# Optimization experiments

Hardware: AMD Instinct MI355X
Metric: run time of the kernel (lower is better)

Reference implementation:

```python
import jax, jax.numpy as jnp
import numpy as np

N_NODES = 50000
HIDDEN = 128
N_EDGES = 1_600_000


def gcn_conv(x, W, b, src, dst, n_nodes):
    """PyG GCNConv: linear, add self-loops, symmetric deg^-1/2 normalization, scatter-sum."""
    h = x @ W  # [N, D]
    # degree with self-loops: 1 + in-degree from edges (edge weight 1)
    deg = jnp.ones((n_nodes,), h.dtype).at[dst].add(1.0)
    dinv = jax.lax.rsqrt(deg)  # deg^{-1/2}, deg >= 1 so no inf
    # neighbor messages: norm_e = dinv[src] * dinv[dst]
    msgs = h[src] * (dinv[src] * dinv[dst])[:, None]  # [E, D]
    agg = jnp.zeros_like(h).at[dst].add(msgs)
    # self-loop contribution: norm = dinv[i]*dinv[i]
    agg = agg + h * (dinv * dinv)[:, None]
    return agg + b


def setup_inputs() -> dict:
    key = jax.random.key(0)
    ks = jax.random.split(key, 7)
    x = jax.random.normal(ks[0], (N_NODES, HIDDEN), dtype=jnp.float32)
    edge_index = jax.random.randint(ks[1], (2, N_EDGES), 0, N_NODES, dtype=jnp.int64)
    s = 1.0 / np.sqrt(HIDDEN)
    W1 = jax.random.uniform(ks[2], (HIDDEN, HIDDEN), jnp.float32, -s, s)
    b1 = jax.random.uniform(ks[3], (HIDDEN,), jnp.float32, -s, s)
    W2 = jax.random.uniform(ks[4], (HIDDEN, HIDDEN), jnp.float32, -s, s)
    b2 = jax.random.uniform(ks[5], (HIDDEN,), jnp.float32, -s, s)
    return {"x": x, "edge_index": edge_index, "W1": W1, "b1": b1, "W2": W2, "b2": b2}


def reference(x, edge_index, W1, b1, W2, b2):
    src, dst = edge_index[0], edge_index[1]
    h = jax.nn.relu(gcn_conv(x, W1, b1, src, dst, N_NODES))
    z = gcn_conv(h, W2, b2, src, dst, N_NODES)
    return z
```

## Files before the change

kernel.cpp:

```cpp
#include <hip/hip_runtime.h>
#include <hip/hip_fp16.h>
#include <type_traits>

#define D 128
#define NI 256
#define MAXNW 25024

using half8 = __attribute__((ext_vector_type(8))) _Float16;
using f32x4 = __attribute__((ext_vector_type(4))) float;


__global__ __launch_bounds__(256) void wprep_kernel(const float* __restrict__ W1,
                                                    const float* __restrict__ W2,
                                                    __half* __restrict__ Wt1,
                                                    __half* __restrict__ Wt2) {
  const float* W = blockIdx.x ? W2 : W1;
  __half* Wt = blockIdx.x ? Wt2 : Wt1;
  for (int idx = threadIdx.x; idx < D * D; idx += 256) {
    int c = idx & 127, k = idx >> 7;
    Wt[c * D + k] = __float2half(W[k * D + c]);
  }
}


__global__ __launch_bounds__(1024) void histA_kernel(const int* __restrict__ dst,
                                                     unsigned short* __restrict__ c,
                                                     unsigned short* __restrict__ rank,
                                                     int E, int N, int CH) {
  __shared__ unsigned int cnt[MAXNW];
  int i = blockIdx.x;
  int nw = (N + 1) >> 1;
  for (int k = threadIdx.x; k < nw; k += 1024) cnt[k] = 0u;
  __syncthreads();
  int e0 = i * CH, e1 = min(e0 + CH, E);
  for (int e = e0 + (int)threadIdx.x; e < e1; e += 1024) {
    int d = dst[e];
    int sh = (d & 1) * 16;
    unsigned int old = atomicAdd(&cnt[d >> 1], 1u << sh);
    rank[e] = (unsigned short)((old >> sh) & 0xffffu);
  }
  __syncthreads();
  unsigned short* ci = c + (size_t)i * N;
  if ((N & 1) == 0) {
    unsigned int* ci32 = reinterpret_cast<unsigned int*>(ci);
    for (int k = threadIdx.x; k < nw; k += 1024) ci32[k] = cnt[k];
  } else {
    for (int k = threadIdx.x; k < nw; k += 1024) {
      unsigned int v = cnt[k];
      int n0 = k * 2;
      ci[n0] = (unsigned short)(v & 0xffffu);
      if (n0 + 1 < N) ci[n0 + 1] = (unsigned short)(v >> 16);
    }
  }
}


__global__ __launch_bounds__(256) void histB_kernel(unsigned short* __restrict__ c,
                                                    int* __restrict__ deg, int N) {
  int n = blockIdx.x * 256 + threadIdx.x;
  if (n >= N) return;
  int run = 0;
  #pragma unroll 8
  for (int i = 0; i < NI; ++i) {
    size_t idx = (size_t)i * N + n;
    int v = c[idx];
    c[idx] = (unsigned short)run;
    run += v;
  }
  deg[n] = run;
}


__global__ __launch_bounds__(256) void bsum_kernel(const int* __restrict__ deg,
                                                   int* __restrict__ bsum) {
  __shared__ int ws[4];
  int i0 = blockIdx.x * 1024 + threadIdx.x * 4;
  int4 v = *reinterpret_cast<const int4*>(deg + i0);
  int s = v.x + v.y + v.z + v.w;
  #pragma unroll
  for (int off = 32; off; off >>= 1) s += __shfl_down(s, off);
  if ((threadIdx.x & 63) == 0) ws[threadIdx.x >> 6] = s;
  __syncthreads();
  if (threadIdx.x == 0) bsum[blockIdx.x] = ws[0] + ws[1] + ws[2] + ws[3];
}


__global__ __launch_bounds__(256) void scan_kernel(const int* __restrict__ deg,
                                                   const int* __restrict__ bsum,
                                                   int* __restrict__ offsets,
                                                   float* __restrict__ dinv,
                                                   int N, int E) {
  __shared__ int ts[256];
  int b = blockIdx.x;
  int base = 0;
  for (int t = 0; t < b; ++t) base += bsum[t];

  int i0 = b * 1024 + threadIdx.x * 4;
  int4 v = *reinterpret_cast<const int4*>(deg + i0);
  int t4 = v.x + v.y + v.z + v.w;
  ts[threadIdx.x] = t4;
  __syncthreads();
  #pragma unroll
  for (int off = 1; off < 256; off <<= 1) {
    int u = (threadIdx.x >= off) ? ts[threadIdx.x - off] : 0;
    __syncthreads();
    ts[threadIdx.x] += u;
    __syncthreads();
  }
  int run = base + ts[threadIdx.x] - t4;

  int dd[4] = {v.x, v.y, v.z, v.w};
  #pragma unroll
  for (int k = 0; k < 4; ++k) {
    int i = i0 + k;
    if (i < N) {
      offsets[i] = run;
      dinv[i] = rsqrtf(1.0f + (float)dd[k]);
    }
    run += dd[k];
  }
  if (b == 0 && threadIdx.x == 0) offsets[N] = E;
}


__global__ __launch_bounds__(256) void place_kernel(const int* __restrict__ src,
                                                    const int* __restrict__ dst,
                                                    const unsigned short* __restrict__ rank,
                                                    const unsigned short* __restrict__ c,
                                                    const int* __restrict__ offsets,
                                                    const float* __restrict__ dinv,
                                                    unsigned int* __restrict__ csr,
                                                    int E, int N, int CH) {
  int t = blockIdx.x * 256 + threadIdx.x;
  int e0 = t * 4;
  if (e0 + 4 <= E) {
    int4 s4 = *reinterpret_cast<const int4*>(src + e0);
    int4 d4 = *reinterpret_cast<const int4*>(dst + e0);
    ushort4 r4 = *reinterpret_cast<const ushort4*>(rank + e0);
    int ss[4] = {s4.x, s4.y, s4.z, s4.w};
    int dd[4] = {d4.x, d4.y, d4.z, d4.w};
    int rr[4] = {r4.x, r4.y, r4.z, r4.w};
    int pos[4];
    float w[4];
    #pragma unroll
    for (int k = 0; k < 4; ++k) {
      int i = (e0 + k) / CH;
      pos[k] = offsets[dd[k]] + (int)c[(size_t)i * N + dd[k]] + rr[k];
    }
    #pragma unroll
    for (int k = 0; k < 4; ++k) w[k] = dinv[ss[k]];
    #pragma unroll
    for (int k = 0; k < 4; ++k) {
      unsigned int q = (unsigned int)__float2int_rn(w[k] * 32767.0f);
      csr[pos[k]] = ((unsigned int)ss[k] << 15) | q;
    }
  } else {
    for (int e = e0; e < E; ++e) {
      int s = src[e];
      int d = dst[e];
      int i = e / CH;
      int pos = offsets[d] + (int)c[(size_t)i * N + d] + (int)rank[e];
      unsigned int q = (unsigned int)__float2int_rn(dinv[s] * 32767.0f);
      csr[pos] = ((unsigned int)s << 15) | q;
    }
  }
}


template <typename TI>
__global__ __launch_bounds__(256) void gemm_mfma_kernel(const TI* __restrict__ X,
                                                        const __half* __restrict__ Wt,
                                                        __half* __restrict__ H, int N) {
  int wid = threadIdx.x >> 6;
  int l = threadIdx.x & 63;
  int row0w = blockIdx.x * 64 + wid * 16;
  int arow = row0w + (l & 15);
  int k0 = (l >> 4) * 8;

  half8 A[4];
  #pragma unroll
  for (int kt = 0; kt < 4; ++kt) {
    half8 a = {};
    if (arow < N) {
      if constexpr (std::is_same<TI, float>::value) {
        const float* p = X + (size_t)arow * D + kt * 32 + k0;
        float4 u = *reinterpret_cast<const float4*>(p);
        float4 v = *reinterpret_cast<const float4*>(p + 4);
        a[0] = (_Float16)u.x; a[1] = (_Float16)u.y;
        a[2] = (_Float16)u.z; a[3] = (_Float16)u.w;
        a[4] = (_Float16)v.x; a[5] = (_Float16)v.y;
        a[6] = (_Float16)v.z; a[7] = (_Float16)v.w;
      } else {
        a = *reinterpret_cast<const half8*>((const __half*)X + (size_t)arow * D + kt * 32 + k0);
      }
    }
    A[kt] = a;
  }

  int wrow = row0w + (l >> 4) * 4;
  int col = l & 15;
  #pragma unroll
  for (int ct = 0; ct < 8; ++ct) {
    f32x4 acc = {0.f, 0.f, 0.f, 0.f};
    #pragma unroll
    for (int kt = 0; kt < 4; ++kt) {
      half8 b = *reinterpret_cast<const half8*>(Wt + (size_t)(ct * 16 + col) * D + kt * 32 + k0);
      acc = __builtin_amdgcn_mfma_f32_16x16x32_f16(A[kt], b, acc, 0, 0, 0);
    }
    #pragma unroll
    for (int r = 0; r < 4; ++r) {
      int row = wrow + r;
      if (row < N) H[(size_t)row * D + ct * 16 + col] = __float2half(acc[r]);
    }
  }
}


template <int DO_RELU, typename TO>
__global__ __launch_bounds__(256) void agg_kernel(const __half* __restrict__ H,
                                                  const int* __restrict__ offsets,
                                                  const unsigned int* __restrict__ csr,
                                                  const float* __restrict__ dinv,
                                                  const float* __restrict__ bias,
                                                  TO* __restrict__ out, int N) {
  int n = blockIdx.x * 4 + (threadIdx.x >> 6);
  if (n >= N) return;
  int lane = threadIdx.x & 63;
  int g = lane >> 4;
  int l = lane & 15;

  int beg = offsets[n];
  int end = offsets[n + 1];

  float acc[8];
  #pragma unroll
  for (int k = 0; k < 8; ++k) acc[k] = 0.f;

  const __half* Hl = H + l * 8;

  int j = beg + g;
  for (; j + 12 < end; j += 16) {
    unsigned int p0 = csr[j];
    unsigned int p1 = csr[j + 4];
    unsigned int p2 = csr[j + 8];
    unsigned int p3 = csr[j + 12];
    float m0 = (float)(p0 & 0x7fffu) * (1.0f / 32767.0f);
    float m1 = (float)(p1 & 0x7fffu) * (1.0f / 32767.0f);
    float m2 = (float)(p2 & 0x7fffu) * (1.0f / 32767.0f);
    float m3 = (float)(p3 & 0x7fffu) * (1.0f / 32767.0f);
    uint4 r0 = *reinterpret_cast<const uint4*>(Hl + (size_t)(p0 >> 15) * D);
    uint4 r1 = *reinterpret_cast<const uint4*>(Hl + (size_t)(p1 >> 15) * D);
    uint4 r2 = *reinterpret_cast<const uint4*>(Hl + (size_t)(p2 >> 15) * D);
    uint4 r3 = *reinterpret_cast<const uint4*>(Hl + (size_t)(p3 >> 15) * D);
    const __half2* h0 = reinterpret_cast<const __half2*>(&r0);
    const __half2* h1 = reinterpret_cast<const __half2*>(&r1);
    const __half2* h2 = reinterpret_cast<const __half2*>(&r2);
    const __half2* h3 = reinterpret_cast<const __half2*>(&r3);
    #pragma unroll
    for (int k = 0; k < 4; ++k) {
      float2 f0 = __half22float2(h0[k]);
      float2 f1 = __half22float2(h1[k]);
      float2 f2 = __half22float2(h2[k]);
      float2 f3 = __half22float2(h3[k]);
      acc[2 * k]     = fmaf(f0.x, m0, acc[2 * k]);
      acc[2 * k + 1] = fmaf(f0.y, m0, acc[2 * k + 1]);
      acc[2 * k]     = fmaf(f1.x, m1, acc[2 * k]);
      acc[2 * k + 1] = fmaf(f1.y, m1, acc[2 * k + 1]);
      acc[2 * k]     = fmaf(f2.x, m2, acc[2 * k]);
      acc[2 * k + 1] = fmaf(f2.y, m2, acc[2 * k + 1]);
      acc[2 * k]     = fmaf(f3.x, m3, acc[2 * k]);
      acc[2 * k + 1] = fmaf(f3.y, m3, acc[2 * k + 1]);
    }
  }
  for (; j < end; j += 4) {
    unsigned int p0 = csr[j];
    float m0 = (float)(p0 & 0x7fffu) * (1.0f / 32767.0f);
    uint4 r0 = *reinterpret_cast<const uint4*>(Hl + (size_t)(p0 >> 15) * D);
    const __half2* h0 = reinterpret_cast<const __half2*>(&r0);
    #pragma unroll
    for (int k = 0; k < 4; ++k) {
      float2 f0 = __half22float2(h0[k]);
      acc[2 * k]     = fmaf(f0.x, m0, acc[2 * k]);
      acc[2 * k + 1] = fmaf(f0.y, m0, acc[2 * k + 1]);
    }
  }

  #pragma unroll
  for (int k = 0; k < 8; ++k) {
    acc[k] += __shfl_xor(acc[k], 16);
    acc[k] += __shfl_xor(acc[k], 32);
  }

  if (g == 0) {
    float di = dinv[n];
    uint4 rs = *reinterpret_cast<const uint4*>(Hl + (size_t)n * D);
    const __half2* hs = reinterpret_cast<const __half2*>(&rs);
    float4 bv0 = *reinterpret_cast<const float4*>(bias + l * 8);
    float4 bv1 = *reinterpret_cast<const float4*>(bias + l * 8 + 4);
    float v[8];
    #pragma unroll
    for (int k = 0; k < 4; ++k) {
      float2 f = __half22float2(hs[k]);
      v[2 * k]     = fmaf(di, fmaf(di, f.x, acc[2 * k]), 0.f);
      v[2 * k + 1] = fmaf(di, fmaf(di, f.y, acc[2 * k + 1]), 0.f);
    }
    v[0] += bv0.x; v[1] += bv0.y; v[2] += bv0.z; v[3] += bv0.w;
    v[4] += bv1.x; v[5] += bv1.y; v[6] += bv1.z; v[7] += bv1.w;
    if (DO_RELU) {
      #pragma unroll
      for (int k = 0; k < 8; ++k) v[k] = fmaxf(v[k], 0.f);
    }
    if constexpr (std::is_same<TO, float>::value) {
      float4 o0 = make_float4(v[0], v[1], v[2], v[3]);
      float4 o1 = make_float4(v[4], v[5], v[6], v[7]);
      *reinterpret_cast<float4*>(out + (size_t)n * D + l * 8) = o0;
      *reinterpret_cast<float4*>(out + (size_t)n * D + l * 8 + 4) = o1;
    } else {
      uint4 pk;
      __half2 q0 = __floats2half2_rn(v[0], v[1]);
      __half2 q1 = __floats2half2_rn(v[2], v[3]);
      __half2 q2 = __floats2half2_rn(v[4], v[5]);
      __half2 q3 = __floats2half2_rn(v[6], v[7]);
      pk.x = *reinterpret_cast<unsigned int*>(&q0);
      pk.y = *reinterpret_cast<unsigned int*>(&q1);
      pk.z = *reinterpret_cast<unsigned int*>(&q2);
      pk.w = *reinterpret_cast<unsigned int*>(&q3);
      *reinterpret_cast<uint4*>((__half*)out + (size_t)n * D + l * 8) = pk;
    }
  }
}


extern "C" void kernel_launch(void* const* d_in, const int* in_sizes, int n_in,
                              void* d_out, int out_size, void* d_ws, size_t ws_size,
                              hipStream_t stream) {
  const float* x  = (const float*)d_in[0];
  const int* edge = (const int*)d_in[1];
  const float* W1 = (const float*)d_in[2];
  const float* b1 = (const float*)d_in[3];
  const float* W2 = (const float*)d_in[4];
  const float* b2 = (const float*)d_in[5];
  const int N = in_sizes[0] / D;
  const int E = in_sizes[1] / 2;
  const int* srcp = edge;
  const int* dstp = edge + E;
  float* out = (float*)d_out;

  const int NP = (N + 1023) & ~1023;
  const int SB = NP / 1024;
  const int CH = (E + NI - 1) / NI;

  auto align = [](size_t v) { return (v + 255) & ~(size_t)255; };
  char* ws = (char*)d_ws;
  size_t o = 0;
  int*   deg     = (int*)(ws + o);             o += align((size_t)NP * 4);
  int*   bsum    = (int*)(ws + o);             o += align((size_t)SB * 4);
  int*   offsets = (int*)(ws + o);             o += align((size_t)(N + 1) * 4);
  float* dinv    = (float*)(ws + o);           o += align((size_t)N * 4);
  unsigned short* c    = (unsigned short*)(ws + o); o += align((size_t)NI * N * 2);
  unsigned short* rank = (unsigned short*)(ws + o); o += align((size_t)((E + 3) & ~3) * 2);
  unsigned int* csr = (unsigned int*)(ws + o); o += align((size_t)E * 4);
  __half* Hh     = (__half*)(ws + o);          o += align((size_t)N * D * 2);
  __half* h1h    = (__half*)(ws + o);          o += align((size_t)N * D * 2);
  __half* Wt1    = (__half*)(ws + o);          o += align((size_t)D * D * 2);
  __half* Wt2    = (__half*)(ws + o);          o += align((size_t)D * D * 2);

  int gemm_blocks = (N + 63) / 64;
  int agg_blocks  = (N + 3) / 4;

  hipMemsetAsync(deg, 0, (size_t)NP * 4, stream);
  wprep_kernel<<<2, 256, 0, stream>>>(W1, W2, Wt1, Wt2);
  histA_kernel<<<NI, 1024, 0, stream>>>(dstp, c, rank, E, N, CH);
  histB_kernel<<<(N + 255) / 256, 256, 0, stream>>>(c, deg, N);
  bsum_kernel<<<SB, 256, 0, stream>>>(deg, bsum);
  scan_kernel<<<SB, 256, 0, stream>>>(deg, bsum, offsets, dinv, N, E);
  int pl_threads = (E + 3) / 4;
  place_kernel<<<(pl_threads + 255) / 256, 256, 0, stream>>>(srcp, dstp, rank, c, offsets,
                                                             dinv, csr, E, N, CH);

  gemm_mfma_kernel<float><<<gemm_blocks, 256, 0, stream>>>(x, Wt1, Hh, N);
  agg_kernel<1, __half><<<agg_blocks, 256, 0, stream>>>(Hh, offsets, csr, dinv, b1, h1h, N);

  gemm_mfma_kernel<__half><<<gemm_blocks, 256, 0, stream>>>(h1h, Wt2, Hh, N);
  agg_kernel<0, float><<<agg_blocks, 256, 0, stream>>>(Hh, offsets, csr, dinv, b2, out, N);
}
```

Before: 265.0 us.

## Halve histogram chunks, fold full edge norm into CSR, drop memset

Halves the number of histogram chunks (NI 256→128), which shrinks the per-chunk count array and the prefix loop in histB. The quantized CSR weight now holds the full dinv[src]*dinv[dst] product, so the aggregation epilogue applies a single self-loop fma instead of a nested outer dinv scale. The deg memset is replaced by histB zeroing the padded tail, and place_kernel computes the chunk index once per 4-edge group. Fewer chunks means more atomic contention per block in histA, and the larger chunks risk overflowing the 16-bit per-chunk counts.

```diff
diff --git a/kernel.cpp b/kernel.cpp
--- a/kernel.cpp
+++ b/kernel.cpp
@@ -3,7 +3,7 @@
 #include <type_traits>
 
 #define D 128
-#define NI 256
+#define NI 128
 #define MAXNW 25024
 
 using half8 = __attribute__((ext_vector_type(8))) _Float16;
@@ -40,25 +40,16 @@
     rank[e] = (unsigned short)((old >> sh) & 0xffffu);
   }
   __syncthreads();
-  unsigned short* ci = c + (size_t)i * N;
-  if ((N & 1) == 0) {
-    unsigned int* ci32 = reinterpret_cast<unsigned int*>(ci);
-    for (int k = threadIdx.x; k < nw; k += 1024) ci32[k] = cnt[k];
-  } else {
-    for (int k = threadIdx.x; k < nw; k += 1024) {
-      unsigned int v = cnt[k];
-      int n0 = k * 2;
-      ci[n0] = (unsigned short)(v & 0xffffu);
-      if (n0 + 1 < N) ci[n0 + 1] = (unsigned short)(v >> 16);
-    }
-  }
+  unsigned int* ci32 = reinterpret_cast<unsigned int*>(c + (size_t)i * N);
+  for (int k = threadIdx.x; k < nw; k += 1024) ci32[k] = cnt[k];
 }
 
 
 __global__ __launch_bounds__(256) void histB_kernel(unsigned short* __restrict__ c,
-                                                    int* __restrict__ deg, int N) {
+                                                    int* __restrict__ deg, int N, int NP) {
   int n = blockIdx.x * 256 + threadIdx.x;
-  if (n >= N) return;
+  if (n >= NP) return;
+  if (n >= N) { deg[n] = 0; return; }
   int run = 0;
   #pragma unroll 8
   for (int i = 0; i < NI; ++i) {
@@ -133,7 +124,9 @@
                                                     int E, int N, int CH) {
   int t = blockIdx.x * 256 + threadIdx.x;
   int e0 = t * 4;
-  if (e0 + 4 <= E) {
+  if (e0 + 4 <= E && (CH & 3) == 0) {
+    int i = e0 / CH;
+    const unsigned short* ci = c + (size_t)i * N;
     int4 s4 = *reinterpret_cast<const int4*>(src + e0);
     int4 d4 = *reinterpret_cast<const int4*>(dst + e0);
     ushort4 r4 = *reinterpret_cast<const ushort4*>(rank + e0);
@@ -141,26 +134,24 @@
     int dd[4] = {d4.x, d4.y, d4.z, d4.w};
     int rr[4] = {r4.x, r4.y, r4.z, r4.w};
     int pos[4];
-    float w[4];
+    float nm[4];
+    #pragma unroll
+    for (int k = 0; k < 4; ++k) pos[k] = offsets[dd[k]] + (int)ci[dd[k]] + rr[k];
+    #pragma unroll
+    for (int k = 0; k < 4; ++k) nm[k] = dinv[ss[k]] * dinv[dd[k]];
     #pragma unroll
     for (int k = 0; k < 4; ++k) {
-      int i = (e0 + k) / CH;
-      pos[k] = offsets[dd[k]] + (int)c[(size_t)i * N + dd[k]] + rr[k];
-    }
-    #pragma unroll
-    for (int k = 0; k < 4; ++k) w[k] = dinv[ss[k]];
-    #pragma unroll
-    for (int k = 0; k < 4; ++k) {
-      unsigned int q = (unsigned int)__float2int_rn(w[k] * 32767.0f);
+      unsigned int q = (unsigned int)__float2int_rn(nm[k] * 32767.0f);
       csr[pos[k]] = ((unsigned int)ss[k] << 15) | q;
     }
   } else {
-    for (int e = e0; e < E; ++e) {
+    for (int e = e0; e < E && e < e0 + 4; ++e) {
       int s = src[e];
       int d = dst[e];
       int i = e / CH;
       int pos = offsets[d] + (int)c[(size_t)i * N + d] + (int)rank[e];
-      unsigned int q = (unsigned int)__float2int_rn(dinv[s] * 32767.0f);
+      float nm = dinv[s] * dinv[d];
+      unsigned int q = (unsigned int)__float2int_rn(nm * 32767.0f);
       csr[pos] = ((unsigned int)s << 15) | q;
     }
   }
@@ -293,6 +284,7 @@
 
   if (g == 0) {
     float di = dinv[n];
+    float dii = di * di;
     uint4 rs = *reinterpret_cast<const uint4*>(Hl + (size_t)n * D);
     const __half2* hs = reinterpret_cast<const __half2*>(&rs);
     float4 bv0 = *reinterpret_cast<const float4*>(bias + l * 8);
@@ -301,8 +293,8 @@
     #pragma unroll
     for (int k = 0; k < 4; ++k) {
       float2 f = __half22float2(hs[k]);
-      v[2 * k]     = fmaf(di, fmaf(di, f.x, acc[2 * k]), 0.f);
-      v[2 * k + 1] = fmaf(di, fmaf(di, f.y, acc[2 * k + 1]), 0.f);
+      v[2 * k]     = fmaf(f.x, dii, acc[2 * k]);
+      v[2 * k + 1] = fmaf(f.y, dii, acc[2 * k + 1]);
     }
     v[0] += bv0.x; v[1] += bv0.y; v[2] += bv0.z; v[3] += bv0.w;
     v[4] += bv1.x; v[5] += bv1.y; v[6] += bv1.z; v[7] += bv1.w;
@@ -368,10 +360,9 @@
   int gemm_blocks = (N + 63) / 64;
   int agg_blocks  = (N + 3) / 4;
 
-  hipMemsetAsync(deg, 0, (size_t)NP * 4, stream);
   wprep_kernel<<<2, 256, 0, stream>>>(W1, W2, Wt1, Wt2);
   histA_kernel<<<NI, 1024, 0, stream>>>(dstp, c, rank, E, N, CH);
-  histB_kernel<<<(N + 255) / 256, 256, 0, stream>>>(c, deg, N);
+  histB_kernel<<<(NP + 255) / 256, 256, 0, stream>>>(c, deg, N, NP);
   bsum_kernel<<<SB, 256, 0, stream>>>(deg, bsum);
   scan_kernel<<<SB, 256, 0, stream>>>(deg, bsum, offsets, dinv, N, E);
   int pl_threads = (E + 3) / 4;
```

Result: faster. 244.5 us (-7.8%).
